# Performance work log

Hardware: AMD Instinct MI355X
Metric: run time of the kernel (lower is better)

The kernel has to match this reference:

```python
import jax, jax.numpy as jnp
import numpy as np

N0, N1, N2, N3 = 600000, 100000, 20000, 4096
E0, E1, E2 = 1500000, 200000, 40960
D_IN, D_H, D_OUT = 100, 256, 47


def setup_inputs() -> dict:
    key = jax.random.key(0)
    ks = jax.random.split(key, 16)
    inp = {
        "x": jax.random.normal(ks[0], (N0, D_IN), jnp.float32),
        "ei0_src": jax.random.randint(ks[1], (E0,), 0, N0, jnp.int32),
        "ei0_dst": jax.random.randint(ks[2], (E0,), 0, N1, jnp.int32),
        "ei1_src": jax.random.randint(ks[3], (E1,), 0, N1, jnp.int32),
        "ei1_dst": jax.random.randint(ks[4], (E1,), 0, N2, jnp.int32),
        "ei2_src": jax.random.randint(ks[5], (E2,), 0, N2, jnp.int32),
        "ei2_dst": jax.random.randint(ks[6], (E2,), 0, N3, jnp.int32),
        "Wl0": jax.random.normal(ks[7], (D_IN, D_H), jnp.float32) * 0.1,
        "Wr0": jax.random.normal(ks[8], (D_IN, D_H), jnp.float32) * 0.1,
        "b0": jnp.zeros((D_H,), jnp.float32),
        "Wl1": jax.random.normal(ks[9], (D_H, D_H), jnp.float32) * 0.06,
        "Wr1": jax.random.normal(ks[10], (D_H, D_H), jnp.float32) * 0.06,
        "b1": jnp.zeros((D_H,), jnp.float32),
        "Wl2": jax.random.normal(ks[11], (D_H, D_OUT), jnp.float32) * 0.06,
        "Wr2": jax.random.normal(ks[12], (D_H, D_OUT), jnp.float32) * 0.06,
        "b2": jnp.zeros((D_OUT,), jnp.float32),
    }
    return inp


def _sage_layer(x_src, x_tgt, src, dst, n_tgt, Wl, Wr, b):
    # PyG SAGEConv (mean aggr): out = lin_l(mean_{j in N(i)} x_j) + lin_r(x_i)
    msgs = x_src[src]                                   # [E, d] gather
    s = jax.ops.segment_sum(msgs, dst, num_segments=n_tgt)
    cnt = jax.ops.segment_sum(jnp.ones((src.shape[0],), x_src.dtype), dst,
                              num_segments=n_tgt)[:, None]
    mean = s / jnp.maximum(cnt, 1.0)
    return mean @ Wl + x_tgt @ Wr + b


def reference(x, ei0_src, ei0_dst, ei1_src, ei1_dst, ei2_src, ei2_dst,
              Wl0, Wr0, b0, Wl1, Wr1, b1, Wl2, Wr2, b2):
    h = _sage_layer(x, x[:N1], ei0_src, ei0_dst, N1, Wl0, Wr0, b0)
    h = jax.nn.relu(h)  # dropout is identity in eval mode
    h = _sage_layer(h, h[:N2], ei1_src, ei1_dst, N2, Wl1, Wr1, b1)
    h = jax.nn.relu(h)
    h = _sage_layer(h, h[:N3], ei2_src, ei2_dst, N3, Wl2, Wr2, b2)
    return jax.nn.log_softmax(h, axis=-1)
```

## Files before the change

### kernel.cpp

```cpp
#include <hip/hip_runtime.h>

#define NN0 600000
#define NN1 100000
#define NN2 20000
#define NN3 4096
#define EE0 1500000
#define EE1 200000
#define EE2 40960
#define DIN 100
#define DH  256
#define DOUT 47
#define NTOT (NN1 + NN2 + NN3)
#define NG 64

#define NB0 98
#define NB1 20
#define NB2 4
#define NBT 122

#define HB0 5860
#define HB1 782
#define HB2 160
#define HBE (HB0 + HB1 + HB2)
#define PACKBLK 108
#define CONVBLK 3072

typedef unsigned int uint;
typedef unsigned short ushort;
typedef __attribute__((ext_vector_type(8))) short bhalf8;
typedef __attribute__((ext_vector_type(4))) float f32x4;

union U16B {
    uint2  u2[2];
    uint4  u4;
    bhalf8 s8;
    ushort us[8];
};

__device__ __forceinline__ ushort f2bf(float f) {
    uint u = __float_as_uint(f);
    uint r = (u + 0x7FFFu + ((u >> 16) & 1u)) >> 16;
    return (ushort)r;
}
__device__ __forceinline__ float bf2f(uint bits16) {
    return __uint_as_float(bits16 << 16);
}

__device__ __forceinline__ void pack_one(const float* B, int K, int N, int NB,
                                         ushort* out, int bid, int l) {
    int kstep = bid / NB;
    int c = bid % NB;
    U16B v;
    #pragma unroll
    for (int j = 0; j < 8; ++j) {
        int k = kstep * 32 + ((l >> 4) << 3) + j;
        int col = (c << 4) | (l & 15);
        float f = (k < K && col < N) ? B[(size_t)k * N + col] : 0.0f;
        v.us[j] = f2bf(f);
    }
    *reinterpret_cast<bhalf8*>(out + ((size_t)bid * 64 + l) * 8) = v.s8;
}

__global__ __launch_bounds__(256)
void hist_conv(const int* __restrict__ e0d, const int* __restrict__ e1d,
               const int* __restrict__ e2d, int* __restrict__ cntp,
               int* __restrict__ pos0, int* __restrict__ pos1, int* __restrict__ pos2,
               const float* __restrict__ x, ushort* __restrict__ xb, long long n4,
               const float* __restrict__ Wl0, const float* __restrict__ Wr0,
               const float* __restrict__ Wl1, const float* __restrict__ Wr1,
               const float* __restrict__ Wl2, const float* __restrict__ Wr2,
               ushort* Bp0l, ushort* Bp0r, ushort* Bp1l, ushort* Bp1r,
               ushort* Bp2l, ushort* Bp2r) {
    int b = blockIdx.x;
    int tid = threadIdx.x;
    if (b < HB0) {
        int e = b * 256 + tid;
        if (e < EE0) {
            int g = b & (NG - 1);
            int p = atomicAdd(&cntp[(size_t)g * NTOT + e0d[e]], 1);
            pos0[e] = p;
        }
    } else if (b < HB0 + HB1) {
        int bb = b - HB0;
        int e = bb * 256 + tid;
        if (e < EE1) {
            int g = bb & (NG - 1);
            int p = atomicAdd(&cntp[(size_t)g * NTOT + NN1 + e1d[e]], 1);
            pos1[e] = p;
        }
    } else if (b < HBE) {
        int bb = b - HB0 - HB1;
        int e = bb * 256 + tid;
        if (e < EE2) {
            int g = bb & (NG - 1);
            int p = atomicAdd(&cntp[(size_t)g * NTOT + NN1 + NN2 + e2d[e]], 1);
            pos2[e] = p;
        }
    } else if (b < HBE + CONVBLK) {
        int cb = b - HBE;
        for (long long t = (long long)cb * 256 + tid; t < n4;
             t += (long long)CONVBLK * 256) {
            float4 v = *reinterpret_cast<const float4*>(x + t * 4);
            uint2 o;
            o.x = (uint)f2bf(v.x) | ((uint)f2bf(v.y) << 16);
            o.y = (uint)f2bf(v.z) | ((uint)f2bf(v.w) << 16);
            *reinterpret_cast<uint2*>(xb + t * 4) = o;
        }
    } else {
        int bid = (b - HBE - CONVBLK) * 4 + (tid >> 6);
        int l = tid & 63;
        if (bid < 64)       pack_one(Wl0, DIN, DH,  16, Bp0l, bid,       l);
        else if (bid < 128) pack_one(Wr0, DIN, DH,  16, Bp0r, bid - 64,  l);
        else if (bid < 256) pack_one(Wl1, DH,  DH,  16, Bp1l, bid - 128, l);
        else if (bid < 384) pack_one(Wr1, DH,  DH,  16, Bp1r, bid - 256, l);
        else if (bid < 408) pack_one(Wl2, DH,  DOUT, 3, Bp2l, bid - 384, l);
        else                pack_one(Wr2, DH,  DOUT, 3, Bp2r, bid - 408, l);
    }
}

__global__ __launch_bounds__(256)
void combine_parts(int* __restrict__ cntp, int* __restrict__ cntAll) {
    int i = blockIdx.x * 256 + threadIdx.x;
    if (i >= NTOT) return;
    int run = 0;
    #pragma unroll 8
    for (int g = 0; g < NG; ++g) {
        size_t idx = (size_t)g * NTOT + i;
        int v = cntp[idx];
        cntp[idx] = run;
        run += v;
    }
    cntAll[i] = run;
}


__device__ __forceinline__ void layer_of(int b, int& lb, int& n, int& po, int& cb) {
    if (b < NB0)      { lb = b;        n = NN1; po = 0;         cb = 0; }
    else if (b < NB0 + NB1) { lb = b - NB0;  n = NN2; po = NB0; cb = NN1; }
    else              { lb = b - NB0 - NB1; n = NN3; po = NB0 + NB1; cb = NN1 + NN2; }
}

__global__ void scan1f(const int* __restrict__ cntAll, int* __restrict__ part) {
    int lb, n, po, cb;
    layer_of(blockIdx.x, lb, n, po, cb);
    __shared__ int s[256];
    int base = lb * 1024;
    int sum = 0;
    for (int i = threadIdx.x; i < 1024; i += 256) {
        int idx = base + i;
        sum += (idx < n) ? cntAll[cb + idx] : 0;
    }
    s[threadIdx.x] = sum;
    __syncthreads();
    for (int off = 128; off; off >>= 1) {
        if (threadIdx.x < off) s[threadIdx.x] += s[threadIdx.x + off];
        __syncthreads();
    }
    if (threadIdx.x == 0) part[po + lb] = s[0];
}

__global__ void scan2f(int* part) {
    __shared__ int s[128];
    int t = threadIdx.x;
    int seg = (t < NB0) ? 0 : (t < NB0 + NB1) ? 1 : (t < NBT) ? 2 : 3;
    int v = (t < NBT) ? part[t] : 0;
    s[t] = v;
    __syncthreads();
    for (int off = 1; off < 128; off <<= 1) {
        int add = 0;
        if (t >= off) {
            int u = t - off;
            int segu = (u < NB0) ? 0 : (u < NB0 + NB1) ? 1 : (u < NBT) ? 2 : 3;
            if (segu == seg) add = s[u];
        }
        __syncthreads();
        s[t] += add;
        __syncthreads();
    }
    if (t < NBT) part[t] = s[t] - v;
}

__global__ void scan3f(const int* __restrict__ cntAll, const int* __restrict__ part,
                       int* __restrict__ rp0, int* __restrict__ rp1,
                       int* __restrict__ rp2) {
    int lb, n, po, cb;
    layer_of(blockIdx.x, lb, n, po, cb);
    int* row_ptr;
    if (cb == 0)        row_ptr = rp0;
    else if (cb == NN1) row_ptr = rp1;
    else                row_ptr = rp2;

    __shared__ int s[256];
    int base = lb * 1024;
    int v[4];
    int sum = 0;
    #pragma unroll
    for (int j = 0; j < 4; ++j) {
        int idx = base + threadIdx.x * 4 + j;
        v[j] = (idx < n) ? cntAll[cb + idx] : 0;
        sum += v[j];
    }
    s[threadIdx.x] = sum;
    __syncthreads();
    for (int off = 1; off < 256; off <<= 1) {
        int t = (threadIdx.x >= off) ? s[threadIdx.x - off] : 0;
        __syncthreads();
        s[threadIdx.x] += t;
        __syncthreads();
    }
    int off0 = part[po + lb] + s[threadIdx.x] - sum;
    #pragma unroll
    for (int j = 0; j < 4; ++j) {
        int idx = base + threadIdx.x * 4 + j;
        if (idx < n) {
            row_ptr[idx] = off0;
            off0 += v[j];
            if (idx == n - 1) row_ptr[n] = off0;
        }
    }
}

__global__ __launch_bounds__(256)
void place_all(const int* __restrict__ e0s, const int* __restrict__ e0d,
               const int* __restrict__ e1s, const int* __restrict__ e1d,
               const int* __restrict__ e2s, const int* __restrict__ e2d,
               const int* __restrict__ pos0, const int* __restrict__ pos1,
               const int* __restrict__ pos2, const int* __restrict__ cntp,
               const int* __restrict__ rp0, const int* __restrict__ rp1,
               const int* __restrict__ rp2,
               int* __restrict__ eidx0, int* __restrict__ eidx1,
               int* __restrict__ eidx2) {
    int b = blockIdx.x;
    int tid = threadIdx.x;
    if (b < HB0) {
        int e = b * 256 + tid;
        if (e < EE0) {
            int d = e0d[e];
            int g = b & (NG - 1);
            int p = rp0[d] + cntp[(size_t)g * NTOT + d] + pos0[e];
            eidx0[p] = e0s[e];
        }
    } else if (b < HB0 + HB1) {
        int bb = b - HB0;
        int e = bb * 256 + tid;
        if (e < EE1) {
            int d = e1d[e];
            int g = bb & (NG - 1);
            int p = rp1[d] + cntp[(size_t)g * NTOT + NN1 + d] + pos1[e];
            eidx1[p] = e1s[e];
        }
    } else {
        int bb = b - HB0 - HB1;
        int e = bb * 256 + tid;
        if (e < EE2) {
            int d = e2d[e];
            int g = bb & (NG - 1);
            int p = rp2[d] + cntp[(size_t)g * NTOT + NN1 + NN2 + d] + pos2[e];
            eidx2[p] = e2s[e];
        }
    }
}


__global__ __launch_bounds__(256)
void agg100_b(const ushort* __restrict__ xb, const int* __restrict__ rp,
              const int* __restrict__ eidx, ushort* __restrict__ out, int nNodes) {
    int node = blockIdx.x * 4 + (threadIdx.x >> 6);
    if (node >= nNodes) return;
    int l = threadIdx.x & 63;
    bool act = l < 50;
    int beg = rp[node], end = rp[node + 1];
    float a0 = 0.f, a1 = 0.f;
    int j = beg;
    for (; j + 3 < end; j += 4) {
        int s0 = eidx[j], s1 = eidx[j + 1], s2 = eidx[j + 2], s3 = eidx[j + 3];
        if (act) {
            uint v0 = *reinterpret_cast<const uint*>(xb + (size_t)s0 * DIN + l * 2);
            uint v1 = *reinterpret_cast<const uint*>(xb + (size_t)s1 * DIN + l * 2);
            uint v2 = *reinterpret_cast<const uint*>(xb + (size_t)s2 * DIN + l * 2);
            uint v3 = *reinterpret_cast<const uint*>(xb + (size_t)s3 * DIN + l * 2);
            a0 += bf2f(v0 & 0xffffu) + bf2f(v1 & 0xffffu) + bf2f(v2 & 0xffffu) + bf2f(v3 & 0xffffu);
            a1 += bf2f(v0 >> 16) + bf2f(v1 >> 16) + bf2f(v2 >> 16) + bf2f(v3 >> 16);
        }
    }
    for (; j < end; ++j) {
        int s0 = eidx[j];
        if (act) {
            uint v0 = *reinterpret_cast<const uint*>(xb + (size_t)s0 * DIN + l * 2);
            a0 += bf2f(v0 & 0xffffu);
            a1 += bf2f(v0 >> 16);
        }
    }
    float inv = 1.0f / fmaxf((float)(end - beg), 1.0f);
    if (act) {
        uint o = (uint)f2bf(a0 * inv) | ((uint)f2bf(a1 * inv) << 16);
        *reinterpret_cast<uint*>(out + (size_t)node * DIN + l * 2) = o;
    }
}

__global__ __launch_bounds__(256)
void agg100_f(const float* __restrict__ x, const int* __restrict__ rp,
              const int* __restrict__ eidx, ushort* __restrict__ out, int nNodes) {
    int node = blockIdx.x * 4 + (threadIdx.x >> 6);
    if (node >= nNodes) return;
    int l = threadIdx.x & 63;
    bool act = l < 50;
    int beg = rp[node], end = rp[node + 1];
    float a0 = 0.f, a1 = 0.f;
    int j = beg;
    for (; j + 1 < end; j += 2) {
        int s0 = eidx[j], s1 = eidx[j + 1];
        if (act) {
            float2 v0 = *reinterpret_cast<const float2*>(x + (size_t)s0 * DIN + l * 2);
            float2 v1 = *reinterpret_cast<const float2*>(x + (size_t)s1 * DIN + l * 2);
            a0 += v0.x + v1.x;
            a1 += v0.y + v1.y;
        }
    }
    if (j < end) {
        int s0 = eidx[j];
        if (act) {
            float2 v0 = *reinterpret_cast<const float2*>(x + (size_t)s0 * DIN + l * 2);
            a0 += v0.x; a1 += v0.y;
        }
    }
    float inv = 1.0f / fmaxf((float)(end - beg), 1.0f);
    if (act) {
        uint o = (uint)f2bf(a0 * inv) | ((uint)f2bf(a1 * inv) << 16);
        *reinterpret_cast<uint*>(out + (size_t)node * DIN + l * 2) = o;
    }
}

__global__ __launch_bounds__(256)
void agg256_b(const ushort* __restrict__ h, const int* __restrict__ rp,
              const int* __restrict__ eidx, ushort* __restrict__ out, int nNodes) {
    int node = blockIdx.x * 4 + (threadIdx.x >> 6);
    if (node >= nNodes) return;
    int l = threadIdx.x & 63;
    int beg = rp[node], end = rp[node + 1];
    float a0 = 0.f, a1 = 0.f, a2 = 0.f, a3 = 0.f;
    int j = beg;
    for (; j + 3 < end; j += 4) {
        int s0 = eidx[j], s1 = eidx[j + 1], s2 = eidx[j + 2], s3 = eidx[j + 3];
        uint2 v0 = *reinterpret_cast<const uint2*>(h + (size_t)s0 * DH + l * 4);
        uint2 v1 = *reinterpret_cast<const uint2*>(h + (size_t)s1 * DH + l * 4);
        uint2 v2 = *reinterpret_cast<const uint2*>(h + (size_t)s2 * DH + l * 4);
        uint2 v3 = *reinterpret_cast<const uint2*>(h + (size_t)s3 * DH + l * 4);
        a0 += bf2f(v0.x & 0xffffu) + bf2f(v1.x & 0xffffu) + bf2f(v2.x & 0xffffu) + bf2f(v3.x & 0xffffu);
        a1 += bf2f(v0.x >> 16)     + bf2f(v1.x >> 16)     + bf2f(v2.x >> 16)     + bf2f(v3.x >> 16);
        a2 += bf2f(v0.y & 0xffffu) + bf2f(v1.y & 0xffffu) + bf2f(v2.y & 0xffffu) + bf2f(v3.y & 0xffffu);
        a3 += bf2f(v0.y >> 16)     + bf2f(v1.y >> 16)     + bf2f(v2.y >> 16)     + bf2f(v3.y >> 16);
    }
    for (; j < end; ++j) {
        int s0 = eidx[j];
        uint2 v0 = *reinterpret_cast<const uint2*>(h + (size_t)s0 * DH + l * 4);
        a0 += bf2f(v0.x & 0xffffu);
        a1 += bf2f(v0.x >> 16);
        a2 += bf2f(v0.y & 0xffffu);
        a3 += bf2f(v0.y >> 16);
    }
    float inv = 1.0f / fmaxf((float)(end - beg), 1.0f);
    uint2 o;
    o.x = (uint)f2bf(a0 * inv) | ((uint)f2bf(a1 * inv) << 16);
    o.y = (uint)f2bf(a2 * inv) | ((uint)f2bf(a3 * inv) << 16);
    *reinterpret_cast<uint2*>(out + (size_t)node * DH + l * 4) = o;
}

template <int RELU, int OUTBF>
__global__ __launch_bounds__(256)
void gemm_dual(const ushort* __restrict__ A1, int K1, int S1, int str1,
               const ushort* __restrict__ A2, int K2, int S2, int str2,
               const ushort* __restrict__ B1p, const ushort* __restrict__ B2p,
               const float* __restrict__ bias, void* __restrict__ Cv,
               int M, int N, int NB, int NBW, int Cstride) {
    __shared__ ushort At[2][2048];

    const int tid = threadIdx.x;
    const int w = tid >> 6;
    const int l = tid & 63;
    const int m0 = blockIdx.x * 64;
    const int S = S1 + S2;

    f32x4 acc[4][4];
    #pragma unroll
    for (int m = 0; m < 4; ++m)
        #pragma unroll
        for (int i = 0; i < 4; ++i)
            acc[m][i] = f32x4{0.f, 0.f, 0.f, 0.f};

    auto stage = [&](int s, int buf) {
        const ushort* A; int str, Keff, ks;
        if (s < S1) { A = A1; str = str1; Keff = K1; ks = s; }
        else        { A = A2; str = str2; Keff = K2; ks = s - S1; }
        int r  = tid >> 2;
        int kc = tid & 3;
        int row = m0 + r;
        int k = ks * 32 + (kc << 3);
        U16B v;
        v.u4.x = v.u4.y = v.u4.z = v.u4.w = 0u;
        if (row < M && k < Keff) {
            const ushort* p = A + (size_t)row * str + k;
            v.u2[0] = *reinterpret_cast<const uint2*>(p);
            v.u2[1] = *reinterpret_cast<const uint2*>(p + 4);
            if (k + 8 > Keff) {
                #pragma unroll
                for (int j = 0; j < 8; ++j)
                    if (k + j >= Keff) v.us[j] = 0;
            }
        }
        int slot = ((r >> 4) << 6) | (r & 15) | (kc << 4);
        *reinterpret_cast<bhalf8*>(&At[buf][slot * 8]) = v.s8;
    };

    stage(0, 0);
    __syncthreads();

    for (int s = 0; s < S; ++s) {
        int buf = s & 1;
        if (s + 1 < S) stage(s + 1, buf ^ 1);

        const ushort* Bp; int ks;
        if (s < S1) { Bp = B1p; ks = s; }
        else        { Bp = B2p; ks = s - S1; }

        bhalf8 a[4];
        #pragma unroll
        for (int m = 0; m < 4; ++m)
            a[m] = *reinterpret_cast<bhalf8*>(&At[buf][((m << 6) | l) * 8]);

        #pragma unroll
        for (int i = 0; i < 4; ++i) {
            if (i < NBW) {
                int c = w * NBW + i;
                if (c < NB) {
                    bhalf8 b = *reinterpret_cast<const bhalf8*>(
                        Bp + ((size_t)(ks * NB + c) * 64 + l) * 8);
                    #pragma unroll
                    for (int m = 0; m < 4; ++m)
                        acc[m][i] = __builtin_amdgcn_mfma_f32_16x16x32_bf16(
                            a[m], b, acc[m][i], 0, 0, 0);
                }
            }
        }
        __syncthreads();
    }

    #pragma unroll
    for (int i = 0; i < 4; ++i) {
        if (i >= NBW) continue;
        int c = w * NBW + i;
        if (c >= NB) continue;
        int col = (c << 4) | (l & 15);
        if (col >= N) continue;
        float bb = bias[col];
        #pragma unroll
        for (int m = 0; m < 4; ++m) {
            #pragma unroll
            for (int e = 0; e < 4; ++e) {
                int row = m0 + (m << 4) + ((l >> 4) << 2) + e;
                if (row < M) {
                    float v = acc[m][i][e] + bb;
                    if (RELU) v = fmaxf(v, 0.0f);
                    if (OUTBF)
                        ((ushort*)Cv)[(size_t)row * Cstride + col] = f2bf(v);
                    else
                        ((float*)Cv)[(size_t)row * Cstride + col] = v;
                }
            }
        }
    }
}

__global__ void log_softmax_47(const float* __restrict__ z, float* __restrict__ out) {
    int row = blockIdx.x;
    int lane = threadIdx.x;
    float v = (lane < DOUT) ? z[(size_t)row * DOUT + lane] : -INFINITY;
    float m = v;
    #pragma unroll
    for (int off = 32; off; off >>= 1) m = fmaxf(m, __shfl_xor(m, off));
    float e = (lane < DOUT) ? expf(v - m) : 0.0f;
    float s = e;
    #pragma unroll
    for (int off = 32; off; off >>= 1) s += __shfl_xor(s, off);
    if (lane < DOUT) out[(size_t)row * DOUT + lane] = v - m - logf(s);
}

extern "C" void kernel_launch(void* const* d_in, const int* in_sizes, int n_in,
                              void* d_out, int out_size, void* d_ws, size_t ws_size,
                              hipStream_t stream) {
    const float* x   = (const float*)d_in[0];
    const int* e0s   = (const int*)d_in[1];
    const int* e0d   = (const int*)d_in[2];
    const int* e1s   = (const int*)d_in[3];
    const int* e1d   = (const int*)d_in[4];
    const int* e2s   = (const int*)d_in[5];
    const int* e2d   = (const int*)d_in[6];
    const float* Wl0 = (const float*)d_in[7];
    const float* Wr0 = (const float*)d_in[8];
    const float* b0  = (const float*)d_in[9];
    const float* Wl1 = (const float*)d_in[10];
    const float* Wr1 = (const float*)d_in[11];
    const float* b1  = (const float*)d_in[12];
    const float* Wl2 = (const float*)d_in[13];
    const float* Wr2 = (const float*)d_in[14];
    const float* b2  = (const float*)d_in[15];

    char* ws = (char*)d_ws;
    size_t off = 0;
    auto alloc = [&](size_t bytes) -> void* {
        void* p = ws + off;
        off += (bytes + 255) & ~(size_t)255;
        return p;
    };

    ushort* agg0b = (ushort*)alloc((size_t)NN1 * DIN * 2);
    ushort* h1    = (ushort*)alloc((size_t)NN1 * DH * 2);
    ushort* agg1b = (ushort*)alloc((size_t)NN2 * DH * 2);
    ushort* h2    = (ushort*)alloc((size_t)NN2 * DH * 2);
    ushort* agg2b = (ushort*)alloc((size_t)NN3 * DH * 2);
    float*  z     = (float*)alloc((size_t)NN3 * DOUT * 4);

    ushort* Bp0l = (ushort*)alloc((size_t)4 * 16 * 64 * 8 * 2);
    ushort* Bp0r = (ushort*)alloc((size_t)4 * 16 * 64 * 8 * 2);
    ushort* Bp1l = (ushort*)alloc((size_t)8 * 16 * 64 * 8 * 2);
    ushort* Bp1r = (ushort*)alloc((size_t)8 * 16 * 64 * 8 * 2);
    ushort* Bp2l = (ushort*)alloc((size_t)8 * 3 * 64 * 8 * 2);
    ushort* Bp2r = (ushort*)alloc((size_t)8 * 3 * 64 * 8 * 2);

    int* cntp   = (int*)alloc((size_t)NG * NTOT * 4);
    int* cntAll = (int*)alloc((size_t)NTOT * 4);
    int* pos0   = (int*)alloc((size_t)EE0 * 4);
    int* pos1   = (int*)alloc((size_t)EE1 * 4);
    int* pos2   = (int*)alloc((size_t)EE2 * 4);
    int* rp0    = (int*)alloc((size_t)(NN1 + 1) * 4);
    int* eidx0  = (int*)alloc((size_t)EE0 * 4);
    int* rp1    = (int*)alloc((size_t)(NN2 + 1) * 4);
    int* eidx1  = (int*)alloc((size_t)EE1 * 4);
    int* rp2    = (int*)alloc((size_t)(NN3 + 1) * 4);
    int* eidx2  = (int*)alloc((size_t)EE2 * 4);
    int* part   = (int*)alloc(256 * 4);

    size_t fullNeed = (size_t)NN0 * DIN * 2 + 4096;
    bool big = (ws_size - off) >= fullNeed;
    int xRows = big ? NN0 : NN1;
    ushort* xb = (ushort*)alloc((size_t)xRows * DIN * 2 + 256);

    hipMemsetAsync(cntp, 0, (size_t)NG * NTOT * 4, stream);
    {
        long long n4 = (long long)xRows * DIN / 4;
        hist_conv<<<HBE + CONVBLK + PACKBLK, 256, 0, stream>>>(
            e0d, e1d, e2d, cntp, pos0, pos1, pos2, x, xb, n4,
            Wl0, Wr0, Wl1, Wr1, Wl2, Wr2,
            Bp0l, Bp0r, Bp1l, Bp1r, Bp2l, Bp2r);
    }

    combine_parts<<<(NTOT + 255) / 256, 256, 0, stream>>>(cntp, cntAll);
    scan1f<<<NBT, 256, 0, stream>>>(cntAll, part);
    scan2f<<<1, 128, 0, stream>>>(part);
    scan3f<<<NBT, 256, 0, stream>>>(cntAll, part, rp0, rp1, rp2);

    place_all<<<HBE, 256, 0, stream>>>(e0s, e0d, e1s, e1d, e2s, e2d,
                                       pos0, pos1, pos2, cntp,
                                       rp0, rp1, rp2, eidx0, eidx1, eidx2);

    if (big)
        agg100_b<<<(NN1 + 3) / 4, 256, 0, stream>>>(xb, rp0, eidx0, agg0b, NN1);
    else
        agg100_f<<<(NN1 + 3) / 4, 256, 0, stream>>>(x, rp0, eidx0, agg0b, NN1);
    gemm_dual<1, 1><<<(NN1 + 63) / 64, 256, 0, stream>>>(
        agg0b, DIN, 4, DIN, xb, DIN, 4, DIN, Bp0l, Bp0r, b0, h1,
        NN1, DH, 16, 4, DH);

    agg256_b<<<(NN2 + 3) / 4, 256, 0, stream>>>(h1, rp1, eidx1, agg1b, NN2);
    gemm_dual<1, 1><<<(NN2 + 63) / 64, 256, 0, stream>>>(
        agg1b, DH, 8, DH, h1, DH, 8, DH, Bp1l, Bp1r, b1, h2,
        NN2, DH, 16, 4, DH);

    agg256_b<<<(NN3 + 3) / 4, 256, 0, stream>>>(h2, rp2, eidx2, agg2b, NN3);
    gemm_dual<0, 0><<<(NN3 + 63) / 64, 256, 0, stream>>>(
        agg2b, DH, 8, DH, h2, DH, 8, DH, Bp2l, Bp2r, b2, z,
        NN3, DOUT, 3, 1, DOUT);

    log_softmax_47<<<NN3, 64, 0, stream>>>(z, (float*)d_out);
}
```

Before: 497.1 us.

## Replace global-atomic degree histogram with LDS-privatized chunked histogram kernel

Edge degree counting moves out of the fused hist_conv kernel into a new hist_lds kernel. Each block takes a contiguous chunk of edges and a 16K-node range and counts with shared-memory atomics, then writes its per-chunk counts to cntp. The memset of cntp goes away and combine_parts/place_all index groups by edge chunk, which cuts global atomic contention. The cost is that each edge chunk is re-read once per node range (7 times for layer 0), and the histogram and convert/pack now run as two launches instead of one.

```diff
diff --git a/kernel.cpp b/kernel.cpp
--- a/kernel.cpp
+++ b/kernel.cpp
@@ -11,7 +11,22 @@
 #define DH  256
 #define DOUT 47
 #define NTOT (NN1 + NN2 + NN3)
-#define NG 64
+
+#define RNG 16384
+#define CH0 32768
+#define NC0 46
+#define R0  7
+#define CH1 16384
+#define NC1 13
+#define R1  2
+#define CH2 8192
+#define NC2 5
+#define R2  1
+#define HL0 (NC0 * R0)
+#define HL1 (NC1 * R1)
+#define HL2 (NC2 * R2)
+#define HLT (HL0 + HL1 + HL2)
+#define NGMAX 46
 
 #define NB0 98
 #define NB1 20
@@ -44,6 +59,47 @@
 }
 __device__ __forceinline__ float bf2f(uint bits16) {
     return __uint_as_float(bits16 << 16);
+}
+
+__global__ __launch_bounds__(256)
+void hist_lds(const int* __restrict__ e0d, const int* __restrict__ e1d,
+              const int* __restrict__ e2d, int* __restrict__ cntp,
+              int* __restrict__ pos0, int* __restrict__ pos1,
+              int* __restrict__ pos2) {
+    __shared__ int lcnt[RNG];
+    int b = blockIdx.x, tid = threadIdx.x;
+    const int* dstp; int E, CH, c, r, nbase, layerN;
+    int* pos;
+    if (b < HL0) {
+        dstp = e0d; E = EE0; CH = CH0; c = b / R0; r = b % R0;
+        nbase = 0; layerN = NN1; pos = pos0;
+    } else if (b < HL0 + HL1) {
+        int bb = b - HL0;
+        dstp = e1d; E = EE1; CH = CH1; c = bb / R1; r = bb % R1;
+        nbase = NN1; layerN = NN2; pos = pos1;
+    } else {
+        int bb = b - HL0 - HL1;
+        dstp = e2d; E = EE2; CH = CH2; c = bb; r = 0;
+        nbase = NN1 + NN2; layerN = NN3; pos = pos2;
+    }
+    for (int i = tid; i < RNG; i += 256) lcnt[i] = 0;
+    __syncthreads();
+    int rbase = r * RNG;
+    long long ebase = (long long)c * CH;
+    for (int i = tid; i < CH; i += 256) {
+        int e = (int)(ebase + i);
+        if (e < E) {
+            int d = dstp[e];
+            unsigned li = (unsigned)(d - rbase);
+            if (li < RNG) pos[e] = atomicAdd(&lcnt[li], 1);
+        }
+    }
+    __syncthreads();
+    for (int i = tid; i < RNG; i += 256) {
+        int node = rbase + i;
+        if (node < layerN)
+            cntp[(size_t)c * NTOT + nbase + node] = lcnt[i];
+    }
 }
 
 __device__ __forceinline__ void pack_one(const float* B, int K, int N, int NB,
@@ -62,10 +118,7 @@
 }
 
 __global__ __launch_bounds__(256)
-void hist_conv(const int* __restrict__ e0d, const int* __restrict__ e1d,
-               const int* __restrict__ e2d, int* __restrict__ cntp,
-               int* __restrict__ pos0, int* __restrict__ pos1, int* __restrict__ pos2,
-               const float* __restrict__ x, ushort* __restrict__ xb, long long n4,
+void conv_pack(const float* __restrict__ x, ushort* __restrict__ xb, long long n4,
                const float* __restrict__ Wl0, const float* __restrict__ Wr0,
                const float* __restrict__ Wl1, const float* __restrict__ Wr1,
                const float* __restrict__ Wl2, const float* __restrict__ Wr2,
@@ -73,32 +126,8 @@
                ushort* Bp2l, ushort* Bp2r) {
     int b = blockIdx.x;
     int tid = threadIdx.x;
-    if (b < HB0) {
-        int e = b * 256 + tid;
-        if (e < EE0) {
-            int g = b & (NG - 1);
-            int p = atomicAdd(&cntp[(size_t)g * NTOT + e0d[e]], 1);
-            pos0[e] = p;
-        }
-    } else if (b < HB0 + HB1) {
-        int bb = b - HB0;
-        int e = bb * 256 + tid;
-        if (e < EE1) {
-            int g = bb & (NG - 1);
-            int p = atomicAdd(&cntp[(size_t)g * NTOT + NN1 + e1d[e]], 1);
-            pos1[e] = p;
-        }
-    } else if (b < HBE) {
-        int bb = b - HB0 - HB1;
-        int e = bb * 256 + tid;
-        if (e < EE2) {
-            int g = bb & (NG - 1);
-            int p = atomicAdd(&cntp[(size_t)g * NTOT + NN1 + NN2 + e2d[e]], 1);
-            pos2[e] = p;
-        }
-    } else if (b < HBE + CONVBLK) {
-        int cb = b - HBE;
-        for (long long t = (long long)cb * 256 + tid; t < n4;
+    if (b < CONVBLK) {
+        for (long long t = (long long)b * 256 + tid; t < n4;
              t += (long long)CONVBLK * 256) {
             float4 v = *reinterpret_cast<const float4*>(x + t * 4);
             uint2 o;
@@ -107,7 +136,7 @@
             *reinterpret_cast<uint2*>(xb + t * 4) = o;
         }
     } else {
-        int bid = (b - HBE - CONVBLK) * 4 + (tid >> 6);
+        int bid = (b - CONVBLK) * 4 + (tid >> 6);
         int l = tid & 63;
         if (bid < 64)       pack_one(Wl0, DIN, DH,  16, Bp0l, bid,       l);
         else if (bid < 128) pack_one(Wr0, DIN, DH,  16, Bp0r, bid - 64,  l);
@@ -122,9 +151,9 @@
 void combine_parts(int* __restrict__ cntp, int* __restrict__ cntAll) {
     int i = blockIdx.x * 256 + threadIdx.x;
     if (i >= NTOT) return;
+    int ng = (i < NN1) ? NC0 : (i < NN1 + NN2) ? NC1 : NC2;
     int run = 0;
-    #pragma unroll 8
-    for (int g = 0; g < NG; ++g) {
+    for (int g = 0; g < ng; ++g) {
         size_t idx = (size_t)g * NTOT + i;
         int v = cntp[idx];
         cntp[idx] = run;
@@ -236,25 +265,23 @@
         int e = b * 256 + tid;
         if (e < EE0) {
             int d = e0d[e];
-            int g = b & (NG - 1);
+            int g = e >> 15;
             int p = rp0[d] + cntp[(size_t)g * NTOT + d] + pos0[e];
             eidx0[p] = e0s[e];
         }
     } else if (b < HB0 + HB1) {
-        int bb = b - HB0;
-        int e = bb * 256 + tid;
+        int e = (b - HB0) * 256 + tid;
         if (e < EE1) {
             int d = e1d[e];
-            int g = bb & (NG - 1);
+            int g = e >> 14;
             int p = rp1[d] + cntp[(size_t)g * NTOT + NN1 + d] + pos1[e];
             eidx1[p] = e1s[e];
         }
     } else {
-        int bb = b - HB0 - HB1;
-        int e = bb * 256 + tid;
+        int e = (b - HB0 - HB1) * 256 + tid;
         if (e < EE2) {
             int d = e2d[e];
-            int g = bb & (NG - 1);
+            int g = e >> 13;
             int p = rp2[d] + cntp[(size_t)g * NTOT + NN1 + NN2 + d] + pos2[e];
             eidx2[p] = e2s[e];
         }
@@ -527,7 +554,7 @@
     ushort* Bp2l = (ushort*)alloc((size_t)8 * 3 * 64 * 8 * 2);
     ushort* Bp2r = (ushort*)alloc((size_t)8 * 3 * 64 * 8 * 2);
 
-    int* cntp   = (int*)alloc((size_t)NG * NTOT * 4);
+    int* cntp   = (int*)alloc((size_t)NGMAX * NTOT * 4);
     int* cntAll = (int*)alloc((size_t)NTOT * 4);
     int* pos0   = (int*)alloc((size_t)EE0 * 4);
     int* pos1   = (int*)alloc((size_t)EE1 * 4);
@@ -545,12 +572,12 @@
     int xRows = big ? NN0 : NN1;
     ushort* xb = (ushort*)alloc((size_t)xRows * DIN * 2 + 256);
 
-    hipMemsetAsync(cntp, 0, (size_t)NG * NTOT * 4, stream);
+    hist_lds<<<HLT, 256, 0, stream>>>(e0d, e1d, e2d, cntp, pos0, pos1, pos2);
+
     {
         long long n4 = (long long)xRows * DIN / 4;
-        hist_conv<<<HBE + CONVBLK + PACKBLK, 256, 0, stream>>>(
-            e0d, e1d, e2d, cntp, pos0, pos1, pos2, x, xb, n4,
-            Wl0, Wr0, Wl1, Wr1, Wl2, Wr2,
+        conv_pack<<<CONVBLK + PACKBLK, 256, 0, stream>>>(
+            x, xb, n4, Wl0, Wr0, Wl1, Wr1, Wl2, Wr2,
             Bp0l, Bp0r, Bp1l, Bp1r, Bp2l, Bp2r);
     }
 
```

Measured after the change: 495.0 us. Within noise of the previous version (-0.4%).
